# Kernel optimization log

Measured on AMD Instinct MI355X. Metric: run time of the kernel, lower is better.

## Reference

```python
import jax, jax.numpy as jnp
import numpy as np

PERSON_DIM = 64
NUM_ZONES = 64
T_STEPS = 65536
N_EDGES = 512
H1, H2 = 128, 64
PENALTY = 1.0  # training_step=0 -> progress=0 -> penalty = min_penalty = 1.0


def build_adjacency(edge_index, num_zones):
    # symmetric 0/1 adjacency with self loops, as in set_graph_data
    A = jnp.zeros((num_zones, num_zones), jnp.float32)
    A = A.at[edge_index[0], edge_index[1]].set(1.0)
    A = A.at[edge_index[1], edge_index[0]].set(1.0)
    return jnp.maximum(A, jnp.eye(num_zones, dtype=jnp.float32))


def setup_inputs() -> dict:
    key = jax.random.key(0)
    ks = jax.random.split(key, 10)
    person_attrs = jax.random.normal(ks[0], (PERSON_DIM,), jnp.float32)
    times = jax.random.uniform(ks[1], (T_STEPS,), jnp.float32)
    zone_features = jax.random.normal(ks[2], (NUM_ZONES, 16), jnp.float32)
    edge_index = jax.random.randint(ks[3], (2, N_EDGES), 0, NUM_ZONES, jnp.int64 if jax.config.jax_enable_x64 else jnp.int32)
    din = PERSON_DIM + 1
    W1 = jax.random.normal(ks[4], (din, H1), jnp.float32) / np.sqrt(din)
    b1 = jnp.zeros((H1,), jnp.float32)
    W2 = jax.random.normal(ks[5], (H1, H2), jnp.float32) / np.sqrt(H1)
    b2 = jnp.zeros((H2,), jnp.float32)
    W3 = jax.random.normal(ks[6], (H2, NUM_ZONES), jnp.float32) / np.sqrt(H2)
    b3 = jnp.zeros((NUM_ZONES,), jnp.float32)
    return {"person_attrs": person_attrs, "times": times, "zone_features": zone_features,
            "edge_index": edge_index, "W1": W1, "b1": b1, "W2": W2, "b2": b2, "W3": W3, "b3": b3}


def reference(person_attrs, times, zone_features, edge_index, W1, b1, W2, b2, W3, b3):
    # MLP input per step = [person_attrs, time]; independent of the recurrence,
    # so batch the 3-layer MLP over all T timesteps (dropout in eval mode = identity).
    T = times.shape[0]
    x = jnp.concatenate([jnp.broadcast_to(person_attrs, (T, person_attrs.shape[0])),
                         times[:, None]], axis=-1)          # [T, D+1]
    h = jax.nn.relu(x @ W1 + b1)                              # [T, 128]
    h = jax.nn.relu(h @ W2 + b2)                              # [T, 64]
    raw_logits = h @ W3 + b3                                  # [T, Z]

    A = build_adjacency(edge_index, raw_logits.shape[-1])

    def step(current_zone, logits):
        constrained = logits - PENALTY * (1.0 - A[current_zone])
        return jnp.argmax(constrained), constrained

    _, zone_logits = jax.lax.scan(step, jnp.asarray(0, jnp.int32), raw_logits)
    return zone_logits  # [T, Z] (original also returns a None placeholder)
```

## Files before the change

kernel.cpp:

```cpp
#include <hip/hip_runtime.h>

#define T_STEPS 65536
#define NZ 64
#define NH1 128
#define NH2 64
#define NEDGE 512
#define NCHUNK 8192
#define CL 8
#define NSUPER 128
#define SUP_L 64
#define STR 67
#define W2STR 68

#define ADJ_OFF        0
#define BASE1_OFF      512
#define W1T_OFF        1536
#define NBRP_OFF       2560
#define DEGS_OFF       6656
#define B2D_OFF        139264
#define B3D_OFF        139776
#define LG32_OFF       140288
#define FTAB_OFF       (LG32_OFF + (size_t)T_STEPS * NZ * 4)
#define CHUNKG_WS      (FTAB_OFF + (size_t)T_STEPS * NZ)
#define SUPERS_WS      (CHUNKG_WS + (size_t)NCHUNK * 64)

typedef unsigned long long ull;
typedef unsigned int u32;
typedef unsigned char u8;
typedef double f64x4 __attribute__((ext_vector_type(4)));
typedef float f32x4 __attribute__((ext_vector_type(4)));

__global__ void prep_kernel(const float* __restrict__ pa,
                            const int* __restrict__ edges,
                            const float* __restrict__ W1,
                            const float* __restrict__ b1,
                            const float* __restrict__ b2,
                            const float* __restrict__ b3,
                            unsigned char* ws) {
  int tid = threadIdx.x;
  if (blockIdx.x == 0) {
    ull* adj = (ull*)(ws + ADJ_OFF);
    if (tid < NZ) adj[tid] = 0ull;
    __syncthreads();
    if (tid < NEDGE) {
      int e0 = edges[tid];
      int e1 = edges[NEDGE + tid];
      atomicOr(&adj[e0], 1ull << e1);
      atomicOr(&adj[e1], 1ull << e0);
    }
    if (tid < NZ) atomicOr(&adj[tid], 1ull << tid);
    __syncthreads();
    if (tid < NZ) {
      ull m = adj[tid];
      u32 wbuf[16];
      #pragma unroll
      for (int i = 0; i < 16; ++i) wbuf[i] = 0u;
      int deg = 0, jfirst = 0;
      while (m) {
        int j = __builtin_ctzll(m);
        m &= m - 1;
        if (deg == 0) jfirst = j;
        wbuf[deg >> 2] |= (u32)j << ((deg & 3) * 8);
        ++deg;
      }
      int padded = (deg + 3) & ~3;
      for (int k = deg; k < padded; ++k)
        wbuf[k >> 2] |= (u32)jfirst << ((k & 3) * 8);
      u32* np = (u32*)(ws + NBRP_OFF) + tid * 16;
      #pragma unroll
      for (int i = 0; i < 16; ++i) np[i] = wbuf[i];
      (ws + DEGS_OFF)[tid] = (u8)(padded >> 2);
    }
  } else {
    double* base1 = (double*)(ws + BASE1_OFF);
    double* w1t   = (double*)(ws + W1T_OFF);
    double* b2d = (double*)(ws + B2D_OFF);
    double* b3d = (double*)(ws + B3D_OFF);
    if (tid < NH1) {
      double acc = (double)b1[tid];
      for (int d = 0; d < 64; ++d)
        acc += (double)pa[d] * (double)W1[d * NH1 + tid];
      base1[tid] = acc;
      w1t[tid] = (double)W1[64 * NH1 + tid];
    }
    if (tid < NH2) b2d[tid] = (double)b2[tid];
    if (tid < NZ)  b3d[tid] = (double)b3[tid];
  }
}

__global__ __launch_bounds__(512, 8) void mlp_tables_kernel(
    const float* __restrict__ times,
    const float* __restrict__ W2,
    const float* __restrict__ W3,
    const unsigned char* __restrict__ ws_ro,
    float* __restrict__ lg32,
    unsigned char* __restrict__ chunkG,
    unsigned char* __restrict__ ftab) {
  __shared__ double region1[4352];
  __shared__ double region2[608];

  float* w2s = (float*)region1;
  double* h2t = region1;
  double* lgT = region1;
  double* base1s = region2;
  double* w1ts = region2 + 128;
  double* pv = region2;
  u8* pi = (u8*)region2 + 4352;
  u8* F_lds = (u8*)region2;

  const double* __restrict__ b2dg = (const double*)(ws_ro + B2D_OFF);
  const double* __restrict__ b3dg = (const double*)(ws_ro + B3D_OFF);

  int tid = threadIdx.x, lane = tid & 63, wv = tid >> 6;
  int i15 = lane & 15, g = lane >> 4;
  int mt = wv & 3, nt0 = (wv >> 2) * 2;
  int t0 = blockIdx.x * 64;

  #pragma unroll
  for (int r = 0; r < 4; ++r) {
    int i = tid + r * 512;
    int row = i >> 4, c4 = (i & 15) << 2;
    *(f32x4*)&w2s[row * W2STR + c4] = *(const f32x4*)&W2[row * 64 + c4];
  }
  if (tid < NH1) {
    base1s[tid] = ((const double*)(ws_ro + BASE1_OFF))[tid];
    w1ts[tid]   = ((const double*)(ws_ro + W1T_OFF))[tid];
  }
  double tv = (double)times[t0 + mt * 16 + i15];
  double bi20 = b2dg[nt0 * 16 + i15], bi21 = b2dg[nt0 * 16 + 16 + i15];
  double bi30 = b3dg[nt0 * 16 + i15], bi31 = b3dg[nt0 * 16 + 16 + i15];
  __syncthreads();

  f64x4 c0, c1;
  c0[0] = bi20; c0[1] = bi20; c0[2] = bi20; c0[3] = bi20;
  c1[0] = bi21; c1[1] = bi21; c1[2] = bi21; c1[3] = bi21;
  #pragma unroll 8
  for (int ks = 0; ks < 32; ++ks) {
    int h = ks * 4 + g;
    double a = fma(tv, w1ts[h], base1s[h]);
    a = a > 0.0 ? a : 0.0;
    double b0 = (double)w2s[h * W2STR + nt0 * 16 + i15];
    double b1 = (double)w2s[h * W2STR + nt0 * 16 + 16 + i15];
    c0 = __builtin_amdgcn_mfma_f64_16x16x4f64(a, b0, c0, 0, 0, 0);
    c1 = __builtin_amdgcn_mfma_f64_16x16x4f64(a, b1, c1, 0, 0, 0);
  }
  __syncthreads();
  #pragma unroll
  for (int r = 0; r < 4; ++r) {
    int t = mt * 16 + g * 4 + r;
    double v0 = c0[r] > 0.0 ? c0[r] : 0.0;
    double v1 = c1[r] > 0.0 ? c1[r] : 0.0;
    h2t[t * STR + nt0 * 16 + i15] = v0;
    h2t[t * STR + nt0 * 16 + 16 + i15] = v1;
  }
  __syncthreads();

  f64x4 d0, d1;
  d0[0] = bi30; d0[1] = bi30; d0[2] = bi30; d0[3] = bi30;
  d1[0] = bi31; d1[1] = bi31; d1[2] = bi31; d1[3] = bi31;
  #pragma unroll 8
  for (int ks = 0; ks < 16; ++ks) {
    int k = ks * 4 + g;
    double a3 = h2t[(mt * 16 + i15) * STR + k];
    double b0 = (double)W3[k * 64 + nt0 * 16 + i15];
    double b1 = (double)W3[k * 64 + nt0 * 16 + 16 + i15];
    d0 = __builtin_amdgcn_mfma_f64_16x16x4f64(a3, b0, d0, 0, 0, 0);
    d1 = __builtin_amdgcn_mfma_f64_16x16x4f64(a3, b1, d1, 0, 0, 0);
  }
  __syncthreads();
  #pragma unroll
  for (int r = 0; r < 4; ++r) {
    int t = mt * 16 + g * 4 + r;
    int z0 = nt0 * 16 + i15, z1 = z0 + 16;
    lgT[z0 * STR + t] = d0[r];
    lgT[z1 * STR + t] = d1[r];
  }
  __syncthreads();

  {
    int zb = wv * 8;
    double vm = lgT[zb * STR + lane];
    int jm = zb;
    lg32[(size_t)zb * T_STEPS + t0 + lane] = (float)vm;
    #pragma unroll
    for (int zz = 1; zz < 8; ++zz) {
      double v = lgT[(zb + zz) * STR + lane];
      lg32[(size_t)(zb + zz) * T_STEPS + t0 + lane] = (float)v;
      if (v > vm) { vm = v; jm = zb + zz; }
    }
    pv[wv * 64 + lane] = vm;
    pi[wv * 64 + lane] = (u8)jm;
  }
  __syncthreads();
  double vmax = pv[lane];
  int jmax = pi[lane];
  #pragma unroll
  for (int w = 1; w < 8; ++w) {
    double v = pv[w * 64 + lane];
    int j = pi[w * 64 + lane];
    if (v > vmax) { vmax = v; jmax = j; }
  }
  double vgap = vmax - 1.0;
  __syncthreads();

  const u32* __restrict__ nbrP = (const u32*)(ws_ro + NBRP_OFF);
  const u8* __restrict__ degs = ws_ro + DEGS_OFF;
  const ull* __restrict__ adjg = (const ull*)(ws_ro + ADJ_OFF);
  #pragma unroll
  for (int zz = 0; zz < 8; ++zz) {
    int z = __builtin_amdgcn_readfirstlane(wv * 8 + zz);
    ull az = adjg[z];
    int nk4 = __builtin_amdgcn_readfirstlane((int)degs[z]);
    double vn = -1.0e300;
    int jn = 0;
    for (int k4 = 0; k4 < nk4; ++k4) {
      u32 w4 = nbrP[z * 16 + k4];
      #pragma unroll
      for (int b = 0; b < 4; ++b) {
        int j = (w4 >> (b * 8)) & 63;
        double val = lgT[j * STR + lane];
        if (val > vn) { vn = val; jn = j; }
      }
    }
    int bit = (int)((az >> jmax) & 1ull);
    int fnb = (vn > vgap) ? jn : ((vn < vgap) ? jmax : (jn < jmax ? jn : jmax));
    F_lds[lane * 68 + z] = (u8)(bit ? jmax : fnb);
  }
  __syncthreads();

  u32* fo = (u32*)(ftab + (size_t)t0 * 64);
  #pragma unroll
  for (int r = 0; r < 2; ++r) {
    int i = tid + r * 512;
    int t = i >> 4, z4 = (i & 15) << 2;
    fo[i] = *(const u32*)&F_lds[t * 68 + z4];
  }

  int c = blockIdx.x * 8 + wv;
  int cur = lane;
  #pragma unroll
  for (int i = 0; i < CL; ++i) cur = F_lds[(wv * 8 + i) * 68 + cur];
  chunkG[(size_t)c * 64 + lane] = (u8)cur;
}

__global__ __launch_bounds__(256) void super_compose_kernel(
    const unsigned char* __restrict__ chunkG,
    unsigned char* __restrict__ superS) {
  __shared__ u8 g[4][SUP_L * 64];
  int tid = threadIdx.x, lane = tid & 63, wv = tid >> 6;
  int k = blockIdx.x * 4 + wv;
  const u32* src = (const u32*)(chunkG + (size_t)k * SUP_L * 64);
  u32* dst = (u32*)g[wv];
  #pragma unroll 4
  for (int i = lane; i < SUP_L * 16; i += 64) dst[i] = src[i];
  int cur = lane;
  #pragma unroll 8
  for (int c = 0; c < SUP_L; ++c) {
    int gg = g[wv][c * 64 + lane];
    cur = __shfl(gg, cur, 64);
  }
  superS[(size_t)k * 64 + lane] = (u8)cur;
}

__global__ __launch_bounds__(256) void states_finalize_kernel(
    const float* __restrict__ lg32, const unsigned char* __restrict__ ws_ro,
    const unsigned char* __restrict__ chunkG,
    const unsigned char* __restrict__ superS,
    const unsigned char* __restrict__ ftab,
    float* __restrict__ out) {
  __shared__ u8 region[NSUPER * 64];
  __shared__ ull adjs[64];
  __shared__ u8 fstage[4][2][CL * 64];
  int tid = threadIdx.x, lane = tid & 63, wv = tid >> 6;
  int b = blockIdx.x;
  int k = b >> 3;
  int myc = b * 8 + wv * 2;

  if (tid < 64) adjs[tid] = ((const ull*)(ws_ro + ADJ_OFF))[tid];
  for (int i = tid; i < NSUPER * 16; i += 256)
    ((u32*)region)[i] = ((const u32*)superS)[i];
  float lgv[2][CL];
  #pragma unroll
  for (int cc = 0; cc < 2; ++cc)
    #pragma unroll
    for (int i = 0; i < CL; ++i)
      lgv[cc][i] = lg32[(size_t)lane * T_STEPS + (myc + cc) * CL + i];
  #pragma unroll
  for (int cc = 0; cc < 2; ++cc)
    for (int i = lane; i < CL * 16; i += 64)
      ((u32*)fstage[wv][cc])[i] =
          ((const u32*)(ftab + (size_t)(myc + cc) * CL * 64))[i];
  __syncthreads();

  int s = 0;
  for (int i = 0; i < k; ++i) s = region[i * 64 + s];
  __syncthreads();
  {
    const u32* cg = (const u32*)(chunkG + (size_t)k * SUP_L * 64);
    for (int i = tid; i < SUP_L * 16; i += 256) ((u32*)region)[i] = cg[i];
  }
  __syncthreads();
  int lc0 = (b & 7) * 8;
  for (int c = 0; c < lc0; ++c) s = region[c * 64 + s];
  int e0 = 0, e1 = 0;
  #pragma unroll
  for (int j = 0; j < 8; ++j) {
    if (j == wv * 2) e0 = s;
    if (j == wv * 2 + 1) e1 = s;
    s = region[(lc0 + j) * 64 + s];
  }

  #pragma unroll
  for (int cc = 0; cc < 2; ++cc) {
    int st = cc ? e1 : e0;
    size_t tb = (size_t)(myc + cc) * CL * 64;
    #pragma unroll
    for (int i = 0; i < CL; ++i) {
      int bit = (int)((adjs[st] >> lane) & 1ull);
      float v = lgv[cc][i];
      out[tb + i * 64 + lane] = bit ? v : v - 1.0f;
      st = fstage[wv][cc][i * 64 + st];
    }
  }
}

extern "C" void kernel_launch(void* const* d_in, const int* in_sizes, int n_in,
                              void* d_out, int out_size, void* d_ws, size_t ws_size,
                              hipStream_t stream) {
  const float* pa    = (const float*)d_in[0];
  const float* times = (const float*)d_in[1];
  const int*   edges = (const int*)d_in[3];
  const float* W1    = (const float*)d_in[4];
  const float* b1    = (const float*)d_in[5];
  const float* W2    = (const float*)d_in[6];
  const float* b2    = (const float*)d_in[7];
  const float* W3    = (const float*)d_in[8];
  const float* b3    = (const float*)d_in[9];

  unsigned char* ws = (unsigned char*)d_ws;
  float* lg32 = (float*)(ws + LG32_OFF);
  unsigned char* ftab = ws + FTAB_OFF;
  unsigned char* chunkG = ws + CHUNKG_WS;
  unsigned char* superS = ws + SUPERS_WS;

  hipLaunchKernelGGL(prep_kernel, dim3(2), dim3(512), 0, stream,
                     pa, edges, W1, b1, b2, b3, ws);
  hipLaunchKernelGGL(mlp_tables_kernel, dim3(T_STEPS / 64), dim3(512), 0, stream,
                     times, W2, W3, ws, lg32, chunkG, ftab);
  hipLaunchKernelGGL(super_compose_kernel, dim3(NSUPER / 4), dim3(256), 0, stream,
                     chunkG, superS);
  hipLaunchKernelGGL(states_finalize_kernel, dim3(NCHUNK / 8), dim3(256), 0, stream,
                     lg32, ws, chunkG, superS, ftab, (float*)d_out);
}
```

Baseline: 77.88 us.

## Fold prep kernel into MLP table kernel, rebuilding adjacency per block

Removes the separate two-block prep launch. Every MLP block now rebuilds the adjacency bitmask in LDS from the edge list with atomics, computes the layer-1 base vector from person attributes itself, and reads the biases directly. Neighbour iteration walks the adjacency bitmask with ctz instead of the packed neighbour list. This saves a launch and the dependency bubble between kernels, at the cost of redundant per-block work: 64x128 W1 reads and LDS atomics in each of 1024 blocks, plus a data-dependent loop.

```diff
diff --git a/kernel.cpp b/kernel.cpp
--- a/kernel.cpp
+++ b/kernel.cpp
@@ -13,12 +13,6 @@
 #define W2STR 68
 
 #define ADJ_OFF        0
-#define BASE1_OFF      512
-#define W1T_OFF        1536
-#define NBRP_OFF       2560
-#define DEGS_OFF       6656
-#define B2D_OFF        139264
-#define B3D_OFF        139776
 #define LG32_OFF       140288
 #define FTAB_OFF       (LG32_OFF + (size_t)T_STEPS * NZ * 4)
 #define CHUNKG_WS      (FTAB_OFF + (size_t)T_STEPS * NZ)
@@ -30,92 +24,47 @@
 typedef double f64x4 __attribute__((ext_vector_type(4)));
 typedef float f32x4 __attribute__((ext_vector_type(4)));
 
-__global__ void prep_kernel(const float* __restrict__ pa,
-                            const int* __restrict__ edges,
-                            const float* __restrict__ W1,
-                            const float* __restrict__ b1,
-                            const float* __restrict__ b2,
-                            const float* __restrict__ b3,
-                            unsigned char* ws) {
-  int tid = threadIdx.x;
-  if (blockIdx.x == 0) {
-    ull* adj = (ull*)(ws + ADJ_OFF);
-    if (tid < NZ) adj[tid] = 0ull;
-    __syncthreads();
-    if (tid < NEDGE) {
-      int e0 = edges[tid];
-      int e1 = edges[NEDGE + tid];
-      atomicOr(&adj[e0], 1ull << e1);
-      atomicOr(&adj[e1], 1ull << e0);
-    }
-    if (tid < NZ) atomicOr(&adj[tid], 1ull << tid);
-    __syncthreads();
-    if (tid < NZ) {
-      ull m = adj[tid];
-      u32 wbuf[16];
-      #pragma unroll
-      for (int i = 0; i < 16; ++i) wbuf[i] = 0u;
-      int deg = 0, jfirst = 0;
-      while (m) {
-        int j = __builtin_ctzll(m);
-        m &= m - 1;
-        if (deg == 0) jfirst = j;
-        wbuf[deg >> 2] |= (u32)j << ((deg & 3) * 8);
-        ++deg;
-      }
-      int padded = (deg + 3) & ~3;
-      for (int k = deg; k < padded; ++k)
-        wbuf[k >> 2] |= (u32)jfirst << ((k & 3) * 8);
-      u32* np = (u32*)(ws + NBRP_OFF) + tid * 16;
-      #pragma unroll
-      for (int i = 0; i < 16; ++i) np[i] = wbuf[i];
-      (ws + DEGS_OFF)[tid] = (u8)(padded >> 2);
-    }
-  } else {
-    double* base1 = (double*)(ws + BASE1_OFF);
-    double* w1t   = (double*)(ws + W1T_OFF);
-    double* b2d = (double*)(ws + B2D_OFF);
-    double* b3d = (double*)(ws + B3D_OFF);
-    if (tid < NH1) {
-      double acc = (double)b1[tid];
-      for (int d = 0; d < 64; ++d)
-        acc += (double)pa[d] * (double)W1[d * NH1 + tid];
-      base1[tid] = acc;
-      w1t[tid] = (double)W1[64 * NH1 + tid];
-    }
-    if (tid < NH2) b2d[tid] = (double)b2[tid];
-    if (tid < NZ)  b3d[tid] = (double)b3[tid];
-  }
-}
-
 __global__ __launch_bounds__(512, 8) void mlp_tables_kernel(
     const float* __restrict__ times,
+    const float* __restrict__ pa,
+    const int* __restrict__ edges,
+    const float* __restrict__ W1,
+    const float* __restrict__ b1,
+    const float* __restrict__ b2,
+    const float* __restrict__ b3,
     const float* __restrict__ W2,
     const float* __restrict__ W3,
-    const unsigned char* __restrict__ ws_ro,
+    unsigned char* __restrict__ ws_adj,
     float* __restrict__ lg32,
     unsigned char* __restrict__ chunkG,
     unsigned char* __restrict__ ftab) {
   __shared__ double region1[4352];
-  __shared__ double region2[608];
+  __shared__ double region2[672];
 
   float* w2s = (float*)region1;
   double* h2t = region1;
   double* lgT = region1;
-  double* base1s = region2;
-  double* w1ts = region2 + 128;
-  double* pv = region2;
-  u8* pi = (u8*)region2 + 4352;
-  u8* F_lds = (u8*)region2;
-
-  const double* __restrict__ b2dg = (const double*)(ws_ro + B2D_OFF);
-  const double* __restrict__ b3dg = (const double*)(ws_ro + B3D_OFF);
+  ull* adj = (ull*)region2;
+  double* base1s = region2 + 64;
+  double* w1ts = region2 + 192;
+  double* pv = region2 + 64;
+  u8* pi = (u8*)region2 + 4608;
+  u8* F_lds = (u8*)region2 + 512;
 
   int tid = threadIdx.x, lane = tid & 63, wv = tid >> 6;
   int i15 = lane & 15, g = lane >> 4;
   int mt = wv & 3, nt0 = (wv >> 2) * 2;
   int t0 = blockIdx.x * 64;
 
+  if (tid < NZ) adj[tid] = 0ull;
+  __syncthreads();
+  {
+    int e0 = edges[tid];
+    int e1 = edges[NEDGE + tid];
+    atomicOr(&adj[e0], 1ull << e1);
+    atomicOr(&adj[e1], 1ull << e0);
+  }
+  if (tid < NZ) atomicOr(&adj[tid], 1ull << tid);
   #pragma unroll
   for (int r = 0; r < 4; ++r) {
     int i = tid + r * 512;
@@ -123,13 +72,19 @@
     *(f32x4*)&w2s[row * W2STR + c4] = *(const f32x4*)&W2[row * 64 + c4];
   }
   if (tid < NH1) {
-    base1s[tid] = ((const double*)(ws_ro + BASE1_OFF))[tid];
-    w1ts[tid]   = ((const double*)(ws_ro + W1T_OFF))[tid];
+    double acc = (double)b1[tid];
+    #pragma unroll 8
+    for (int d = 0; d < 64; ++d)
+      acc += (double)pa[d] * (double)W1[d * NH1 + tid];
+    base1s[tid] = acc;
+    w1ts[tid] = (double)W1[64 * NH1 + tid];
   }
   double tv = (double)times[t0 + mt * 16 + i15];
-  double bi20 = b2dg[nt0 * 16 + i15], bi21 = b2dg[nt0 * 16 + 16 + i15];
-  double bi30 = b3dg[nt0 * 16 + i15], bi31 = b3dg[nt0 * 16 + 16 + i15];
-  __syncthreads();
+  double bi20 = (double)b2[nt0 * 16 + i15], bi21 = (double)b2[nt0 * 16 + 16 + i15];
+  double bi30 = (double)b3[nt0 * 16 + i15], bi31 = (double)b3[nt0 * 16 + 16 + i15];
+  __syncthreads();
+
+  if (blockIdx.x == 0 && tid < NZ) ((ull*)ws_adj)[tid] = adj[tid];
 
   f64x4 c0, c1;
   c0[0] = bi20; c0[1] = bi20; c0[2] = bi20; c0[3] = bi20;
@@ -140,9 +95,9 @@
     double a = fma(tv, w1ts[h], base1s[h]);
     a = a > 0.0 ? a : 0.0;
     double b0 = (double)w2s[h * W2STR + nt0 * 16 + i15];
-    double b1 = (double)w2s[h * W2STR + nt0 * 16 + 16 + i15];
+    double b1v = (double)w2s[h * W2STR + nt0 * 16 + 16 + i15];
     c0 = __builtin_amdgcn_mfma_f64_16x16x4f64(a, b0, c0, 0, 0, 0);
-    c1 = __builtin_amdgcn_mfma_f64_16x16x4f64(a, b1, c1, 0, 0, 0);
+    c1 = __builtin_amdgcn_mfma_f64_16x16x4f64(a, b1v, c1, 0, 0, 0);
   }
   __syncthreads();
   #pragma unroll
@@ -163,9 +118,9 @@
     int k = ks * 4 + g;
     double a3 = h2t[(mt * 16 + i15) * STR + k];
     double b0 = (double)W3[k * 64 + nt0 * 16 + i15];
-    double b1 = (double)W3[k * 64 + nt0 * 16 + 16 + i15];
+    double b1v = (double)W3[k * 64 + nt0 * 16 + 16 + i15];
     d0 = __builtin_amdgcn_mfma_f64_16x16x4f64(a3, b0, d0, 0, 0, 0);
-    d1 = __builtin_amdgcn_mfma_f64_16x16x4f64(a3, b1, d1, 0, 0, 0);
+    d1 = __builtin_amdgcn_mfma_f64_16x16x4f64(a3, b1v, d1, 0, 0, 0);
   }
   __syncthreads();
   #pragma unroll
@@ -203,24 +158,20 @@
   double vgap = vmax - 1.0;
   __syncthreads();
 
-  const u32* __restrict__ nbrP = (const u32*)(ws_ro + NBRP_OFF);
-  const u8* __restrict__ degs = ws_ro + DEGS_OFF;
-  const ull* __restrict__ adjg = (const ull*)(ws_ro + ADJ_OFF);
   #pragma unroll
   for (int zz = 0; zz < 8; ++zz) {
     int z = __builtin_amdgcn_readfirstlane(wv * 8 + zz);
-    ull az = adjg[z];
-    int nk4 = __builtin_amdgcn_readfirstlane((int)degs[z]);
+    ull az = adj[z];
+    u32 mlo = __builtin_amdgcn_readfirstlane((u32)az);
+    u32 mhi = __builtin_amdgcn_readfirstlane((u32)(az >> 32));
+    ull m = ((ull)mhi << 32) | mlo;
     double vn = -1.0e300;
     int jn = 0;
-    for (int k4 = 0; k4 < nk4; ++k4) {
-      u32 w4 = nbrP[z * 16 + k4];
-      #pragma unroll
-      for (int b = 0; b < 4; ++b) {
-        int j = (w4 >> (b * 8)) & 63;
-        double val = lgT[j * STR + lane];
-        if (val > vn) { vn = val; jn = j; }
-      }
+    while (m) {
+      int j = __builtin_ctzll(m);
+      m &= m - 1;
+      double val = lgT[j * STR + lane];
+      if (val > vn) { vn = val; jn = j; }
     }
     int bit = (int)((az >> jmax) & 1ull);
     int fnb = (vn > vgap) ? jn : ((vn < vgap) ? jmax : (jn < jmax ? jn : jmax));
@@ -343,10 +294,9 @@
   unsigned char* chunkG = ws + CHUNKG_WS;
   unsigned char* superS = ws + SUPERS_WS;
 
-  hipLaunchKernelGGL(prep_kernel, dim3(2), dim3(512), 0, stream,
-                     pa, edges, W1, b1, b2, b3, ws);
   hipLaunchKernelGGL(mlp_tables_kernel, dim3(T_STEPS / 64), dim3(512), 0, stream,
-                     times, W2, W3, ws, lg32, chunkG, ftab);
+                     times, pa, edges, W1, b1, b2, b3, W2, W3,
+                     ws + ADJ_OFF, lg32, chunkG, ftab);
   hipLaunchKernelGGL(super_compose_kernel, dim3(NSUPER / 4), dim3(256), 0, stream,
                      chunkG, superS);
   hipLaunchKernelGGL(states_finalize_kernel, dim3(NCHUNK / 8), dim3(256), 0, stream,
```

Result: faster. 75.60 us (-2.9%).
